# Kernel tuning notes

Measured on AMD Instinct MI355X. Metric: run time of the kernel, lower is better.

Reference implementation:

```python
import jax, jax.numpy as jnp
import numpy as np

MUL = 50        # e3nn mul=50 channel multiplicity
LAYERS = 6      # layers=6
NBASIS = 10     # radial basis size
MAXR = 0.06     # max_radius
HIDDEN = 64     # radial MLP hidden
NPATHS = 5      # TP paths: s*Y0->s, s*Y1->v, v.Y1->s, vxY1->v, Y2@v->v
HALF_BAR = 0.05 # half bar length (bar lengths [0.1,0.1,0.1])


def setup_inputs() -> dict:
    key = jax.random.key(0)
    ks = jax.random.split(key, 9)
    B, L = 64, 514
    C = MUL
    y = jax.random.normal(ks[0], (B, L, 6), dtype=jnp.float32) * 0.03
    W_embed = jax.random.normal(ks[1], (3, C), dtype=jnp.float32) / np.sqrt(3.0)
    Wr1 = jax.random.normal(ks[2], (LAYERS, NBASIS + 2, HIDDEN), dtype=jnp.float32) / np.sqrt(NBASIS + 2.0)
    br1 = jnp.zeros((LAYERS, HIDDEN), dtype=jnp.float32)
    Wr2 = jax.random.normal(ks[3], (LAYERS, HIDDEN, NPATHS * C), dtype=jnp.float32) / np.sqrt(float(HIDDEN))
    Ws = jax.random.normal(ks[4], (LAYERS, C, C), dtype=jnp.float32) / np.sqrt(float(C))
    Wv = jax.random.normal(ks[5], (LAYERS, C, C), dtype=jnp.float32) / np.sqrt(float(C))
    Wg = jax.random.normal(ks[6], (LAYERS, C, C), dtype=jnp.float32) / np.sqrt(float(C))
    W_out = jax.random.normal(ks[7], (C,), dtype=jnp.float32) / np.sqrt(float(C))
    return {"y": y, "W_embed": W_embed, "Wr1": Wr1, "br1": br1, "Wr2": Wr2,
            "Ws": Ws, "Wv": Wv, "Wg": Wg, "W_out": W_out}


def _cross2d(a, b):
    return a[..., 0] * b[..., 1] - a[..., 1] * b[..., 0]


def _forward(y, W_embed, Wr1, br1, Wr2, Ws, Wv, Wg, W_out):
    B, L, _ = y.shape
    T = L - 2
    C = MUL
    # --- slinky coord transform: (x, z, alpha) dof -> 9 cartesian points/triplet ---
    ctr = jnp.stack([y[..., 0], y[..., 1]], axis=-1)                 # (B,L,2) bar centers
    a = y[..., 2]
    off = HALF_BAR * jnp.stack([-jnp.sin(a), jnp.cos(a)], axis=-1)   # (B,L,2)
    pts = jnp.stack([ctr + off, ctr, ctr - off], axis=-2)            # (B,L,3,2) top/center/bottom
    trip = jnp.stack([pts[:, :-2], pts[:, 1:-1], pts[:, 2:]], axis=2)  # (B,T,3bars,3pts,2)
    cart = trip.reshape(B * T, 9, 2)
    nt = B * T
    N = nt * 9
    pos = jnp.concatenate([cart.reshape(-1, 2), jnp.zeros((N, 1), cart.dtype)], axis=-1)  # (N,3)
    # --- fixed intra-triplet edge pattern ---
    base = jnp.array([[1, 0], [1, 2], [4, 3], [4, 5], [7, 6], [7, 8], [1, 4], [4, 7]], dtype=jnp.int32)
    eidx = (base[None] + 9 * jnp.arange(nt, dtype=jnp.int32)[:, None, None]).reshape(-1, 2)
    src, dst = eidx[:, 0], eidx[:, 1]
    edge_attr = jnp.tile(jax.nn.one_hot(jnp.array([1, 1, 1, 1, 1, 1, 0, 0]), 2, dtype=pos.dtype), (nt, 1))  # (E,2)
    node_attr = jnp.tile(jax.nn.one_hot(jnp.array([1, 0, 1]), 2, dtype=pos.dtype), (3 * nt, 1))             # (N,2)
    node_input = jnp.ones((N, 1), pos.dtype)
    # --- edge geometry: radial embedding + spherical harmonics l<=2 ---
    edge_vec = pos[src] - pos[dst]
    r = jnp.linalg.norm(edge_vec, axis=-1)
    u = edge_vec / (r[:, None] + 1e-12)                              # Y1 (l=1)
    centers = jnp.linspace(0.0, MAXR, NBASIS)
    width = MAXR / (NBASIS - 1)
    rb = jnp.exp(-jnp.square((r[:, None] - centers) / width))        # (E,NBASIS)
    t = jnp.clip(r / MAXR, 0.0, 1.0)
    fcut = 0.5 * (jnp.cos(jnp.float32(np.pi) * t) + 1.0)             # smooth cutoff at max_radius
    emb = jnp.concatenate([rb * fcut[:, None], edge_attr], axis=-1)  # (E,NBASIS+2)
    Y2 = u[:, :, None] * u[:, None, :] - jnp.eye(3, dtype=u.dtype) / 3.0  # traceless l=2 (E,3,3)
    # --- node feature init: scalars (0e) + zero vectors (1o) ---
    s = jnp.concatenate([node_input, node_attr], axis=-1) @ W_embed  # (N,C)
    v = jnp.zeros((N, C, 3), pos.dtype)
    for l in range(LAYERS):
        w = jax.nn.silu(emb @ Wr1[l] + br1[l]) @ Wr2[l]              # radial MLP -> TP weights
        w = w.reshape(-1, NPATHS, C) * fcut[:, None, None]           # (E,5,C)
        ss, vs = s[src], v[src]
        m_s = w[:, 0] * ss + w[:, 2] * jnp.einsum('ecd,ed->ec', vs, u)
        m_v = (w[:, 1, :, None] * ss[:, :, None] * u[:, None, :]
               + w[:, 3, :, None] * jnp.cross(vs, u[:, None, :])
               + w[:, 4, :, None] * jnp.einsum('ecd,edk->eck', vs, Y2))
        s_agg = jax.ops.segment_sum(m_s, dst, num_segments=N)        # scatter-add (num_neighbors=1)
        v_agg = jax.ops.segment_sum(m_v, dst, num_segments=N)
        h = s + s_agg
        s = jax.nn.silu(h @ Ws[l])                                   # scalar nonlinearity
        gate = jax.nn.sigmoid(h @ Wg[l])                             # equivariant gate for vectors
        v = jnp.einsum('ncd,ck->nkd', v + v_agg, Wv[l]) * gate[:, :, None]
    out = jnp.einsum('ncd,c->nd', v, W_out)                          # 1x1o readout, (N,3)
    output = out.reshape(B, T, 3, 3, 3)                              # (B,T,bar,point,xyz)
    cart_b = cart.reshape(B, T, 3, 3, 2)
    result = jnp.zeros((B, L, 3), y.dtype)
    result = result.at[:, 1:-1, 0:2].set(output.sum(axis=-2)[..., 1, 0:2])
    tmp = (_cross2d(cart_b[..., 0, :] - cart_b[..., 1, :], output[..., 0, 0:2])
           + _cross2d(cart_b[..., 2, :] - cart_b[..., 1, :], output[..., 2, 0:2]))
    result = result.at[:, 1:-1, 2].set(tmp[..., 1])
    return result


def reference(y, W_embed, Wr1, br1, Wr2, Ws, Wv, Wg, W_out):
    return _forward(y, W_embed, Wr1, br1, Wr2, Ws, Wv, Wg, W_out)
```

## Files before the change

### kernel.cpp

```cpp
#include <hip/hip_runtime.h>
#include <math.h>

#define PI_F 3.14159265358979323846f

typedef _Float16 h8 __attribute__((ext_vector_type(8)));
typedef float f4 __attribute__((ext_vector_type(4)));

__device__ __forceinline__ float sigm_(float x){ return 1.0f/(1.0f+__expf(-x)); }
__device__ __forceinline__ float silu_(float x){ return x*sigm_(x); }
__device__ __forceinline__ h8 ldh8(const _Float16* p){
    return __builtin_bit_cast(h8, *(const float4*)(p));
}

#define B1_PER_L 21504
#define B2_PER_L 12288
#define B1_TOT   129024
#define B_TOT    202752

#define AROWS 104

__global__ void precompute_k1(const float* __restrict__ W_embed,
                              const float* __restrict__ Wr1,
                              const float* __restrict__ br1,
                              const float* __restrict__ Wr2,
                              const float* __restrict__ Ws,
                              const float* __restrict__ Wg,
                              const float* __restrict__ Wv,
                              float* __restrict__ pre,
                              float* __restrict__ T,
                              int tabN,
                              _Float16* __restrict__ B,
                              float* __restrict__ out,
                              int nTb)
{
    const int bid = blockIdx.x;
    const int tid = threadIdx.x;
    const float wdt = 0.06f / 9.0f;

    if (bid == 0) {
        for (int i = tid; i < 384; i += 256) {
            int b = i / 6, r = i - b * 6;
            int t = (r < 3) ? 0 : 513;
            out[((size_t)(b * 514 + t)) * 3 + (r % 3)] = 0.0f;
        }
        __shared__ float s1[50];
        __shared__ float hid[64];
        if (tid < 50) s1[tid] = W_embed[tid] + W_embed[50 + tid];
        __syncthreads();

        const float rbar = 0.05f;
        const float fcb = 0.5f * (__cosf(PI_F * (rbar / 0.06f)) + 1.0f);
        float emb[12];
#pragma unroll
        for (int i = 0; i < 10; ++i) {
            float d = (rbar - (float)i * wdt) / wdt;
            emb[i] = __expf(-d * d) * fcb;
        }
        emb[10] = 0.0f; emb[11] = 1.0f;

        for (int l = 0; l < 6; ++l) {
            if (tid < 50) pre[l * 50 + tid] = s1[tid];
            if (tid < 64) {
                float a = br1[l * 64 + tid];
#pragma unroll
                for (int i = 0; i < 12; ++i) a += emb[i] * Wr1[l * 768 + i * 64 + tid];
                hid[tid] = silu_(a);
            }
            __syncthreads();
            for (int m = tid; m < 250; m += 256) {
                float acc = 0.0f;
                for (int j = 0; j < 64; ++j) acc += hid[j] * Wr2[l * 16000 + j * 250 + m];
                pre[300 + l * 250 + m] = acc * fcb;
            }
            float sacc = 0.0f;
            if (tid < 50) {
                for (int c = 0; c < 50; ++c) sacc += s1[c] * Ws[l * 2500 + c * 50 + tid];
            }
            __syncthreads();
            if (tid < 50) s1[tid] = silu_(sacc);
            __syncthreads();
        }
    } else if (bid <= nTb) {
        const int e = (bid - 1) * 4 + (tid >> 6);
        const int lane = tid & 63;
        const int total = 6 * (tabN + 1);
        if (e >= total) return;
        const int l = e / (tabN + 1);
        const int i = e - l * (tabN + 1);

        float r = (float)i * (0.06f / (float)tabN);
        float t = fminf(r * (1.0f / 0.06f), 1.0f);
        float fc = 0.5f * (__cosf(PI_F * t) + 1.0f);
        float emb[10];
#pragma unroll
        for (int k = 0; k < 10; ++k) {
            float d = (r - (float)k * wdt) / wdt;
            emb[k] = __expf(-d * d) * fc;
        }
        float a = br1[l * 64 + lane] + Wr1[l * 768 + 640 + lane];
#pragma unroll
        for (int k = 0; k < 10; ++k) a += emb[k] * Wr1[l * 768 + k * 64 + lane];
        float hv = silu_(a);

        float acc0 = 0.0f, acc1 = 0.0f;
        const float* wr2 = Wr2 + l * 16000;
        for (int j = 0; j < 64; ++j) {
            float hj = __shfl(hv, j);
            acc0 += hj * wr2[j * 250 + lane];
            acc1 += hj * wr2[j * 250 + 64 + lane];
        }
        float* tp = T + (size_t)e * 100;
        float sh0 = __shfl(acc0, lane + 50);
        float sh1 = __shfl(acc1, lane - 14);
        float vb = ((lane < 14) ? sh0 : sh1) * fc;
        if (lane < 50) *(float2*)(tp + 2 * lane) = make_float2(acc0 * fc, vb);
    } else {
        int idx = (bid - 1 - nTb) * 256 + tid;
        if (idx >= B_TOT) return;
        int l, n, k, which;
        size_t off;
        if (idx < B1_TOT) {
            l = idx / B1_PER_L; int r = idx - l * B1_PER_L;
            n = r / 192; k = r - n * 192; which = 0;
            off = (size_t)l * B1_PER_L + n * 192 + k;
        } else {
            int j = idx - B1_TOT;
            l = j / B2_PER_L; int r = j - l * B2_PER_L;
            n = r / 192; k = r - n * 192; which = 1;
            off = B1_TOT + (size_t)l * B2_PER_L + n * 192 + k;
        }
        int seg = -1, c = 0;
        if (k < 50)                  { seg = 0; c = k; }
        else if (k >= 64 && k < 114) { seg = 1; c = k - 64; }
        else if (k >= 128 && k < 178){ seg = 2; c = k - 128; }
        _Float16 val = (_Float16)0.0f;
        if (seg >= 0) {
            float w = 0.0f;
            if (which == 0) {
                if (n < 50)       w = Ws[l * 2500 + c * 50 + n];
                else if (n < 100) w = Wg[l * 2500 + c * 50 + (n - 50)];
            } else {
                if (n < 50)       w = Wv[l * 2500 + c * 50 + n];
            }
            _Float16 hi = (_Float16)w;
            val = (seg < 2) ? hi : (_Float16)(w - (float)hi);
        }
        B[off] = val;
    }
}

__global__ __launch_bounds__(256, 4)
void fused_k2(const float* __restrict__ y,
              const float* __restrict__ W_embed,
              const float* __restrict__ W_out,
              const float* __restrict__ pre,
              const float* __restrict__ T,
              int tabN,
              const _Float16* __restrict__ Bws,
              float* __restrict__ out)
{
    __shared__ __align__(16) char LB[AROWS * 128 * 2];
    _Float16* A   = (_Float16*)LB;
    float* outHT  = (float*)LB;
    float* outQT  = (float*)LB + 2400;

    const int tid  = threadIdx.x;
    const int wave = tid >> 6;
    const int lane = tid & 63;
    const int kl   = (lane < 50) ? lane : 49;
    const int fm   = lane & 15;
    const int fq   = lane >> 4;

    const _Float16* B1 = Bws;
    const _Float16* B2 = Bws + B1_TOT;

    float offx[2], offy[2], u3x_[2], u3y_[2], uspx_[2], uspy_[2], fr_[2];
    int   ti_[2], inr_[2];
#pragma unroll
    for (int w = 0; w < 2; ++w) {
        int wid = blockIdx.x * 8 + wave * 2 + w;
        int b = wid >> 9, tw = wid & 511;
        const float* yb = y + ((size_t)(b * 514 + tw)) * 6;
        float c0x = yb[0], c0y = yb[1];
        float c1x = yb[6], c1y = yb[7], a1 = yb[8];
        float sn, cs; __sincosf(a1, &sn, &cs);
        offx[w] = -0.05f * sn; offy[w] = 0.05f * cs;
        float svx = c0x - c1x, svy = c0y - c1y;
        float r_sp = sqrtf(svx * svx + svy * svy);
        float inv_sp = 1.0f / (r_sp + 1e-12f);
        uspx_[w] = svx * inv_sp; uspy_[w] = svy * inv_sp;
        float rb2 = sqrtf(offx[w] * offx[w] + offy[w] * offy[w]);
        float invb = 1.0f / (rb2 + 1e-12f);
        u3x_[w] = -offx[w] * invb; u3y_[w] = -offy[w] * invb;
        float tp = r_sp * ((float)tabN / 0.06f);
        inr_[w] = tp < (float)tabN;
        int ti = (int)tp;
        if (ti > tabN - 1) ti = tabN - 1;
        if (ti < 0) ti = 0;
        ti_[w] = ti; fr_[w] = tp - (float)ti;
    }

    float s3[2], s4[2], s5[2];
    float v3x[2], v3y[2], v3z[2], v4x[2], v4y[2], v4z[2], v5x[2], v5y[2], v5z[2];
    {
        float i35 = W_embed[kl] + W_embed[100 + kl];
        float i4  = W_embed[kl] + W_embed[50 + kl];
#pragma unroll
        for (int w = 0; w < 2; ++w) {
            s3[w] = i35; s5[w] = i35; s4[w] = i4;
            v3x[w] = v3y[w] = v3z[w] = 0.0f;
            v4x[w] = v4y[w] = v4z[w] = 0.0f;
            v5x[w] = v5y[w] = v5z[w] = 0.0f;
        }
    }

    for (int l = 0; l < 6; ++l) {
        __syncthreads();

        float s1l = pre[l * 50 + kl];
        const float* wbp = pre + 300 + l * 250;
        float wb0 = wbp[kl], wb1 = wbp[50 + kl], wb2 = wbp[100 + kl],
              wb3 = wbp[150 + kl], wb4 = wbp[200 + kl];

        const float THIRD = 1.0f / 3.0f;
#pragma unroll
        for (int w = 0; w < 2; ++w) {
            const float* tb = T + ((size_t)(l * (tabN + 1) + ti_[w])) * 100 + 2 * kl;
            float2 t0 = *(const float2*)tb;
            float2 t1 = *(const float2*)(tb + 100);
            float wsp0 = inr_[w] ? (t0.x + fr_[w] * (t1.x - t0.x)) : 0.0f;
            float wsp1 = inr_[w] ? (t0.y + fr_[w] * (t1.y - t0.y)) : 0.0f;

            float u3x = u3x_[w], u3y = u3y_[w];
            float dot3 = v4x[w] * u3x + v4y[w] * u3y;
            float ms3 = wb0 * s4[w] + wb2 * dot3;
            float ms5 = wb0 * s4[w] - wb2 * dot3;
            float ms4 = wsp0 * s1l;
            float bAx = wb1 * s4[w] * u3x - wb3 * v4z[w] * u3y;
            float bAy = wb1 * s4[w] * u3y + wb3 * v4z[w] * u3x;
            float bBx = wb4 * (dot3 * u3x - v4x[w] * THIRD);
            float bBy = wb4 * (dot3 * u3y - v4y[w] * THIRD);
            float crz = wb3 * (v4x[w] * u3y - v4y[w] * u3x);
            float mzc = -wb4 * v4z[w] * THIRD;

            float vals[12];
            vals[0] = s3[w] + ms3;
            vals[1] = s4[w] + ms4;
            vals[2] = s5[w] + ms5;
            vals[3] = v3x[w] + bAx + bBx;
            vals[4] = v3y[w] + bAy + bBy;
            vals[5] = v3z[w] + crz + mzc;
            vals[6] = v4x[w] + wsp1 * s1l * uspx_[w];
            vals[7] = v4y[w] + wsp1 * s1l * uspy_[w];
            vals[8] = v4z[w];
            vals[9]  = v5x[w] - bAx + bBx;
            vals[10] = v5y[w] - bAy + bBy;
            vals[11] = v5z[w] - crz + mzc;

            int wv = wave * 2 + w;
#pragma unroll
            for (int q = 0; q < 12; ++q) {
                int row = (q < 3) ? (wv * 3 + q) : (24 + wv * 9 + (q - 3));
                float x = (lane < 50) ? vals[q] : 0.0f;
                _Float16 hi = (_Float16)x;
                _Float16 lo = (_Float16)(x - (float)hi);
                int col = lane ^ ((row & 7) << 3);
                A[row * 128 + col]      = hi;
                A[row * 128 + col + 64] = lo;
            }
        }
        __syncthreads();

        f4 cst[9];
        const _Float16* B1l = B1 + (size_t)l * B1_PER_L;
        const _Float16* B2l = B2 + (size_t)l * B2_PER_L;

        {
            const _Float16* bp = B1l + (wave * 16 + fm) * 192 + fq * 8;
            h8 b0 = ldh8(bp), b1 = ldh8(bp + 32), b2 = ldh8(bp + 64),
               b3 = ldh8(bp + 96), b4 = ldh8(bp + 128), b5 = ldh8(bp + 160);
#pragma unroll
            for (int mt = 0; mt < 2; ++mt) {
                const int row = mt * 16 + fm;
                const int x32 = (row & 4) << 3;
                const _Float16* ap = A + row * 128 + ((fq ^ (row & 3)) << 3);
                h8 a0 = ldh8(ap + x32);
                h8 a1 = ldh8(ap + 32 - x32);
                h8 a2 = ldh8(ap + 64 + x32);
                h8 a3 = ldh8(ap + 96 - x32);
                f4 acc = {0.0f, 0.0f, 0.0f, 0.0f};
                acc = __builtin_amdgcn_mfma_f32_16x16x32_f16(a0, b0, acc, 0, 0, 0);
                acc = __builtin_amdgcn_mfma_f32_16x16x32_f16(a1, b1, acc, 0, 0, 0);
                acc = __builtin_amdgcn_mfma_f32_16x16x32_f16(a2, b2, acc, 0, 0, 0);
                acc = __builtin_amdgcn_mfma_f32_16x16x32_f16(a3, b3, acc, 0, 0, 0);
                acc = __builtin_amdgcn_mfma_f32_16x16x32_f16(a0, b4, acc, 0, 0, 0);
                acc = __builtin_amdgcn_mfma_f32_16x16x32_f16(a1, b5, acc, 0, 0, 0);
                cst[mt] = acc;
            }
        }
        if (wave < 3) {
            const _Float16* bp = B1l + ((4 + wave) * 16 + fm) * 192 + fq * 8;
            h8 b0 = ldh8(bp), b1 = ldh8(bp + 32), b2 = ldh8(bp + 64),
               b3 = ldh8(bp + 96), b4 = ldh8(bp + 128), b5 = ldh8(bp + 160);
#pragma unroll
            for (int mt = 0; mt < 2; ++mt) {
                const int row = mt * 16 + fm;
                const int x32 = (row & 4) << 3;
                const _Float16* ap = A + row * 128 + ((fq ^ (row & 3)) << 3);
                h8 a0 = ldh8(ap + x32);
                h8 a1 = ldh8(ap + 32 - x32);
                h8 a2 = ldh8(ap + 64 + x32);
                h8 a3 = ldh8(ap + 96 - x32);
                f4 acc = {0.0f, 0.0f, 0.0f, 0.0f};
                acc = __builtin_amdgcn_mfma_f32_16x16x32_f16(a0, b0, acc, 0, 0, 0);
                acc = __builtin_amdgcn_mfma_f32_16x16x32_f16(a1, b1, acc, 0, 0, 0);
                acc = __builtin_amdgcn_mfma_f32_16x16x32_f16(a2, b2, acc, 0, 0, 0);
                acc = __builtin_amdgcn_mfma_f32_16x16x32_f16(a3, b3, acc, 0, 0, 0);
                acc = __builtin_amdgcn_mfma_f32_16x16x32_f16(a0, b4, acc, 0, 0, 0);
                acc = __builtin_amdgcn_mfma_f32_16x16x32_f16(a1, b5, acc, 0, 0, 0);
                cst[2 + mt] = acc;
            }
        }
        {
            const _Float16* bp = B2l + (wave * 16 + fm) * 192 + fq * 8;
            h8 b0 = ldh8(bp), b1 = ldh8(bp + 32), b2 = ldh8(bp + 64),
               b3 = ldh8(bp + 96), b4 = ldh8(bp + 128), b5 = ldh8(bp + 160);
#pragma unroll
            for (int mt = 0; mt < 5; ++mt) {
                const int row = 24 + mt * 16 + fm;
                const int x32 = (row & 4) << 3;
                const _Float16* ap = A + row * 128 + ((fq ^ (row & 3)) << 3);
                h8 a0 = ldh8(ap + x32);
                h8 a1 = ldh8(ap + 32 - x32);
                h8 a2 = ldh8(ap + 64 + x32);
                h8 a3 = ldh8(ap + 96 - x32);
                f4 acc = {0.0f, 0.0f, 0.0f, 0.0f};
                acc = __builtin_amdgcn_mfma_f32_16x16x32_f16(a0, b0, acc, 0, 0, 0);
                acc = __builtin_amdgcn_mfma_f32_16x16x32_f16(a1, b1, acc, 0, 0, 0);
                acc = __builtin_amdgcn_mfma_f32_16x16x32_f16(a2, b2, acc, 0, 0, 0);
                acc = __builtin_amdgcn_mfma_f32_16x16x32_f16(a3, b3, acc, 0, 0, 0);
                acc = __builtin_amdgcn_mfma_f32_16x16x32_f16(a0, b4, acc, 0, 0, 0);
                acc = __builtin_amdgcn_mfma_f32_16x16x32_f16(a1, b5, acc, 0, 0, 0);
                cst[4 + mt] = acc;
            }
        }
        __syncthreads();

        {
            int n0 = wave * 16 + fm;
#pragma unroll
            for (int mt = 0; mt < 2; ++mt)
#pragma unroll
                for (int i = 0; i < 4; ++i) {
                    int r = mt * 16 + fq * 4 + i;
                    if (r < 24) outHT[r * 100 + n0] = cst[mt][i];
                }
            if (wave < 3) {
                int n1 = (4 + wave) * 16 + fm;
                if (n1 < 100) {
#pragma unroll
                    for (int mt = 0; mt < 2; ++mt)
#pragma unroll
                        for (int i = 0; i < 4; ++i) {
                            int r = mt * 16 + fq * 4 + i;
                            if (r < 24) outHT[r * 100 + n1] = cst[2 + mt][i];
                        }
                }
            }
            if (n0 < 50) {
#pragma unroll
                for (int mt = 0; mt < 5; ++mt)
#pragma unroll
                    for (int i = 0; i < 4; ++i) {
                        int r = mt * 16 + fq * 4 + i;
                        if (r < 72) outQT[r * 50 + n0] = cst[4 + mt][i];
                    }
            }
        }
        __syncthreads();

#pragma unroll
        for (int w = 0; w < 2; ++w) {
            int wv = wave * 2 + w;
            int mb = wv * 3, qb = wv * 9;
            float as3 = outHT[(mb    ) * 100 + kl];
            float as4 = outHT[(mb + 1) * 100 + kl];
            float as5 = outHT[(mb + 2) * 100 + kl];
            float ag3 = outHT[(mb    ) * 100 + 50 + kl];
            float ag4 = outHT[(mb + 1) * 100 + 50 + kl];
            float ag5 = outHT[(mb + 2) * 100 + 50 + kl];
            float g3 = sigm_(ag3), g4 = sigm_(ag4), g5 = sigm_(ag5);
            s3[w] = silu_(as3); s4[w] = silu_(as4); s5[w] = silu_(as5);
            v3x[w] = outQT[(qb    ) * 50 + kl] * g3;
            v3y[w] = outQT[(qb + 1) * 50 + kl] * g3;
            v3z[w] = outQT[(qb + 2) * 50 + kl] * g3;
            v4x[w] = outQT[(qb + 3) * 50 + kl] * g4;
            v4y[w] = outQT[(qb + 4) * 50 + kl] * g4;
            v4z[w] = outQT[(qb + 5) * 50 + kl] * g4;
            v5x[w] = outQT[(qb + 6) * 50 + kl] * g5;
            v5y[w] = outQT[(qb + 7) * 50 + kl] * g5;
            v5z[w] = outQT[(qb + 8) * 50 + kl] * g5;
        }
    }

    float wo = (lane < 50) ? W_out[lane] : 0.0f;
#pragma unroll
    for (int w = 0; w < 2; ++w) {
        float px  = (v3x[w] + v4x[w] + v5x[w]) * wo;
        float py  = (v3y[w] + v4y[w] + v5y[w]) * wo;
        float dxv = (v3x[w] - v5x[w]) * wo;
        float dyv = (v3y[w] - v5y[w]) * wo;
#pragma unroll
        for (int o = 32; o > 0; o >>= 1) {
            px  += __shfl_xor(px, o);
            py  += __shfl_xor(py, o);
            dxv += __shfl_xor(dxv, o);
            dyv += __shfl_xor(dyv, o);
        }
        if (lane == 0) {
            int wid = blockIdx.x * 8 + wave * 2 + w;
            int b = wid >> 9, tw = wid & 511;
            float* op = out + ((size_t)(b * 514 + (tw + 1))) * 3;
            op[0] = px;
            op[1] = py;
            op[2] = offx[w] * dyv - offy[w] * dxv;
        }
    }
}

extern "C" void kernel_launch(void* const* d_in, const int* in_sizes, int n_in,
                              void* d_out, int out_size, void* d_ws, size_t ws_size,
                              hipStream_t stream) {
    const float* y       = (const float*)d_in[0];
    const float* W_embed = (const float*)d_in[1];
    const float* Wr1     = (const float*)d_in[2];
    const float* br1     = (const float*)d_in[3];
    const float* Wr2     = (const float*)d_in[4];
    const float* Ws      = (const float*)d_in[5];
    const float* Wv      = (const float*)d_in[6];
    const float* Wg      = (const float*)d_in[7];
    const float* W_out   = (const float*)d_in[8];
    float* out = (float*)d_out;

    _Float16* Bws = (_Float16*)d_ws;
    float* pre = (float*)((char*)d_ws + B_TOT * 2);
    float* T   = pre + 1800;

    int tabN = 1024;
    while (tabN > 64 &&
           (size_t)B_TOT * 2 + (size_t)(1800 + 6 * (tabN + 1) * 100) * sizeof(float) > ws_size)
        tabN >>= 1;

    int nTb = (6 * (tabN + 1) + 3) / 4;
    int nFb = (B_TOT + 255) / 256;
    precompute_k1<<<1 + nTb + nFb, 256, 0, stream>>>(
        W_embed, Wr1, br1, Wr2, Ws, Wg, Wv, pre, T, tabN, Bws, out, nTb);
    fused_k2<<<4096, 256, 0, stream>>>(y, W_embed, W_out, pre, T, tabN, Bws, out);
}
```

Baseline: 346.7 us.

## Split A and output LDS buffers to drop two barriers per layer

Gives the fp16 A operand and the fp32 output transpose staging separate LDS regions instead of aliasing them, so the barrier at loop top and the barrier between MFMA reads and output writes can be removed. It also replaces the XOR swizzle of A with a padded row stride of 136 halves to avoid bank conflicts more simply. The cost is about 52 KB of shared memory per block instead of about 26 KB, which can lower the 4-blocks-per-CU occupancy, and correctness now depends on the remaining barriers still ordering every cross-wave hazard.

Result: faster. 317.4 us (-8.5%).

```diff
diff --git a/kernel.cpp b/kernel.cpp
--- a/kernel.cpp
+++ b/kernel.cpp
@@ -17,7 +17,8 @@
 #define B1_TOT   129024
 #define B_TOT    202752
 
-#define AROWS 104
+#define ASTR 136
+#define A_BYTES 28288
 
 __global__ void precompute_k1(const float* __restrict__ W_embed,
                               const float* __restrict__ Wr1,
@@ -159,10 +160,10 @@
               const _Float16* __restrict__ Bws,
               float* __restrict__ out)
 {
-    __shared__ __align__(16) char LB[AROWS * 128 * 2];
+    __shared__ __align__(16) char LB[A_BYTES + 24000];
     _Float16* A   = (_Float16*)LB;
-    float* outHT  = (float*)LB;
-    float* outQT  = (float*)LB + 2400;
+    float* outHT  = (float*)(LB + A_BYTES);
+    float* outQT  = (float*)(LB + A_BYTES) + 2400;
 
     const int tid  = threadIdx.x;
     const int wave = tid >> 6;
@@ -215,8 +216,6 @@
     }
 
     for (int l = 0; l < 6; ++l) {
-        __syncthreads();
-
         float s1l = pre[l * 50 + kl];
         const float* wbp = pre + 300 + l * 250;
         float wb0 = wbp[kl], wb1 = wbp[50 + kl], wb2 = wbp[100 + kl],
@@ -264,9 +263,8 @@
                 float x = (lane < 50) ? vals[q] : 0.0f;
                 _Float16 hi = (_Float16)x;
                 _Float16 lo = (_Float16)(x - (float)hi);
-                int col = lane ^ ((row & 7) << 3);
-                A[row * 128 + col]      = hi;
-                A[row * 128 + col + 64] = lo;
+                A[row * ASTR + lane]      = hi;
+                A[row * ASTR + 64 + lane] = lo;
             }
         }
         __syncthreads();
@@ -281,13 +279,8 @@
                b3 = ldh8(bp + 96), b4 = ldh8(bp + 128), b5 = ldh8(bp + 160);
 #pragma unroll
             for (int mt = 0; mt < 2; ++mt) {
-                const int row = mt * 16 + fm;
-                const int x32 = (row & 4) << 3;
-                const _Float16* ap = A + row * 128 + ((fq ^ (row & 3)) << 3);
-                h8 a0 = ldh8(ap + x32);
-                h8 a1 = ldh8(ap + 32 - x32);
-                h8 a2 = ldh8(ap + 64 + x32);
-                h8 a3 = ldh8(ap + 96 - x32);
+                const _Float16* ap = A + (mt * 16 + fm) * ASTR + fq * 8;
+                h8 a0 = ldh8(ap), a1 = ldh8(ap + 32), a2 = ldh8(ap + 64), a3 = ldh8(ap + 96);
                 f4 acc = {0.0f, 0.0f, 0.0f, 0.0f};
                 acc = __builtin_amdgcn_mfma_f32_16x16x32_f16(a0, b0, acc, 0, 0, 0);
                 acc = __builtin_amdgcn_mfma_f32_16x16x32_f16(a1, b1, acc, 0, 0, 0);
@@ -304,13 +297,8 @@
                b3 = ldh8(bp + 96), b4 = ldh8(bp + 128), b5 = ldh8(bp + 160);
 #pragma unroll
             for (int mt = 0; mt < 2; ++mt) {
-                const int row = mt * 16 + fm;
-                const int x32 = (row & 4) << 3;
-                const _Float16* ap = A + row * 128 + ((fq ^ (row & 3)) << 3);
-                h8 a0 = ldh8(ap + x32);
-                h8 a1 = ldh8(ap + 32 - x32);
-                h8 a2 = ldh8(ap + 64 + x32);
-                h8 a3 = ldh8(ap + 96 - x32);
+                const _Float16* ap = A + (mt * 16 + fm) * ASTR + fq * 8;
+                h8 a0 = ldh8(ap), a1 = ldh8(ap + 32), a2 = ldh8(ap + 64), a3 = ldh8(ap + 96);
                 f4 acc = {0.0f, 0.0f, 0.0f, 0.0f};
                 acc = __builtin_amdgcn_mfma_f32_16x16x32_f16(a0, b0, acc, 0, 0, 0);
                 acc = __builtin_amdgcn_mfma_f32_16x16x32_f16(a1, b1, acc, 0, 0, 0);
@@ -327,13 +315,8 @@
                b3 = ldh8(bp + 96), b4 = ldh8(bp + 128), b5 = ldh8(bp + 160);
 #pragma unroll
             for (int mt = 0; mt < 5; ++mt) {
-                const int row = 24 + mt * 16 + fm;
-                const int x32 = (row & 4) << 3;
-                const _Float16* ap = A + row * 128 + ((fq ^ (row & 3)) << 3);
-                h8 a0 = ldh8(ap + x32);
-                h8 a1 = ldh8(ap + 32 - x32);
-                h8 a2 = ldh8(ap + 64 + x32);
-                h8 a3 = ldh8(ap + 96 - x32);
+                const _Float16* ap = A + (24 + mt * 16 + fm) * ASTR + fq * 8;
+                h8 a0 = ldh8(ap), a1 = ldh8(ap + 32), a2 = ldh8(ap + 64), a3 = ldh8(ap + 96);
                 f4 acc = {0.0f, 0.0f, 0.0f, 0.0f};
                 acc = __builtin_amdgcn_mfma_f32_16x16x32_f16(a0, b0, acc, 0, 0, 0);
                 acc = __builtin_amdgcn_mfma_f32_16x16x32_f16(a1, b1, acc, 0, 0, 0);
@@ -344,7 +327,6 @@
                 cst[4 + mt] = acc;
             }
         }
-        __syncthreads();
 
         {
             int n0 = wave * 16 + fm;
```
